# Kernel optimization log

Hardware: AMD Instinct MI355X
Metric: run time of the kernel (lower is better)

Reference implementation:

```python
import jax, jax.numpy as jnp
import numpy as np

N, T, F, H, DEG = 1024, 32, 128, 4, 32
HID, OUT = 512, 64
NNZ = N * DEG
D = F // H


def setup_inputs() -> dict:
    key = jax.random.key(0)
    ks = jax.random.split(key, 40)
    p = lambda i, shape, s=0.05: (jax.random.normal(ks[i], shape, dtype=jnp.float32) * s)
    inp = {
        'A_rows': jnp.repeat(jnp.arange(N, dtype=jnp.int32), DEG),
        'A_cols': jax.random.randint(ks[0], (NNZ,), 0, N, dtype=jnp.int32),
        'A_vals': jax.random.uniform(ks[1], (NNZ,), dtype=jnp.float32) / DEG,
        'X': jax.random.normal(ks[2], (N, T, F), dtype=jnp.float32),
        'W_gcn': p(3, (F, F)),
        'W_ih': p(4, (3 * F, F)), 'W_hh': p(5, (3 * F, F)),
        'b_ih': p(6, (3 * F,)), 'b_hh': p(7, (3 * F,)),
        'in_proj_w': p(8, (3 * F, F)), 'in_proj_b': p(9, (3 * F,)),
        'out_proj_w': p(10, (F, F)), 'out_proj_b': p(11, (F,)),
        'ln1_g': jnp.ones((F,), jnp.float32), 'ln1_b': jnp.zeros((F,), jnp.float32),
        'ln2_g': jnp.ones((F,), jnp.float32), 'ln2_b': jnp.zeros((F,), jnp.float32),
        'lnf_g': jnp.ones((F,), jnp.float32), 'lnf_b': jnp.zeros((F,), jnp.float32),
        'ff1_w': p(12, (HID, F)), 'ff1_b': p(13, (HID,)),
        'ff2_w': p(14, (F, HID)), 'ff2_b': p(15, (F,)),
        'fc1_w': p(16, (HID, T * F)), 'fc1_b': p(17, (HID,)),
        'fc2_w': p(18, (HID, HID)), 'fc2_b': p(19, (HID,)),
        'fc3_w': p(20, (OUT, HID)), 'fc3_b': p(21, (OUT,)),
    }
    return inp


def _pos_encoding():
    # pe[i, t] = sin(t / 10000**(2i/F)) for even t, cos(...) for odd t; constant over feature dim.
    i = jnp.arange(N, dtype=jnp.float32)
    t = jnp.arange(T, dtype=jnp.float32)
    inv = jnp.exp(-(2.0 * i / F) * jnp.log(jnp.float32(10000.0)))  # [N]
    ang = t[None, :] * inv[:, None]                                # [N, T]
    even = (jnp.arange(T) % 2 == 0)[None, :]
    return jnp.where(even, jnp.sin(ang), jnp.cos(ang))             # [N, T]


def _layer_norm(x, g, b, eps=1e-5):
    mu = x.mean(-1, keepdims=True)
    var = ((x - mu) ** 2).mean(-1, keepdims=True)
    return (x - mu) * jax.lax.rsqrt(var + eps) * g + b


def _forward(A_rows, A_cols, A_vals, X, W_gcn, W_ih, W_hh, b_ih, b_hh,
             in_proj_w, in_proj_b, out_proj_w, out_proj_b,
             ln1_g, ln1_b, ln2_g, ln2_b, lnf_g, lnf_b,
             ff1_w, ff1_b, ff2_w, ff2_b,
             fc1_w, fc1_b, fc2_w, fc2_b, fc3_w, fc3_b):
    def spmm(x2d):  # A_hat @ x2d via COO gather + segment-sum
        return jax.ops.segment_sum(A_vals[:, None] * x2d[A_cols], A_rows, num_segments=N)

    def gru_cell(x, h):  # torch GRUCell, gate order [r; z; n]
        gi = x @ W_ih.T + b_ih
        gh = h @ W_hh.T + b_hh
        ir, iz, inn = jnp.split(gi, 3, axis=-1)
        hr, hz, hn = jnp.split(gh, 3, axis=-1)
        r = jax.nn.sigmoid(ir + hr)
        z = jax.nn.sigmoid(iz + hz)
        n = jnp.tanh(inn + r * hn)
        return (1.0 - z) * n + z * h

    # GCN on full [N, T, F] block
    X_tilde = jax.nn.relu(spmm(X.reshape(N, T * F)).reshape(N, T, F) @ W_gcn)

    # sequential GRU + per-step GCN over time
    def step(h, x_t):
        g = gru_cell(x_t, h)                       # [N, F]
        h_new = jax.nn.relu(spmm(g) @ W_gcn)
        return h_new, g

    h0 = jnp.zeros((N, F), X.dtype)
    _, Hs = jax.lax.scan(step, h0, jnp.transpose(X_tilde, (1, 0, 2)))  # [T, N, F]
    Hm = jnp.transpose(Hs, (1, 0, 2)) + _pos_encoding()[:, :, None]    # [N, T, F]

    # TransformerEncoderLayer (post-norm, relu, dropout=0); seq axis = nodes, batch axis = T
    qkv = Hm @ in_proj_w.T + in_proj_b                 # [N, T, 3F]
    q, k, v = jnp.split(qkv, 3, axis=-1)
    q = q.reshape(N, T, H, D) * (1.0 / jnp.sqrt(jnp.float32(D)))
    k = k.reshape(N, T, H, D)
    v = v.reshape(N, T, H, D)
    scores = jnp.einsum('nthd,mthd->thnm', q, k)       # [T, H, N, N]
    attn = jax.nn.softmax(scores, axis=-1)
    ctx = jnp.einsum('thnm,mthd->nthd', attn, v).reshape(N, T, F)
    attn_out = ctx @ out_proj_w.T + out_proj_b
    x1 = _layer_norm(Hm + attn_out, ln1_g, ln1_b)
    ff = jax.nn.relu(x1 @ ff1_w.T + ff1_b) @ ff2_w.T + ff2_b
    x2 = _layer_norm(x1 + ff, ln2_g, ln2_b)
    enc = _layer_norm(x2, lnf_g, lnf_b)                # final encoder norm

    # MLP head
    flat = enc.reshape(N, T * F)
    h1 = jax.nn.relu(flat @ fc1_w.T + fc1_b)
    h2 = jax.nn.relu(h1 @ fc2_w.T + fc2_b)
    return h2 @ fc3_w.T + fc3_b                        # [N, OUT]


def reference(A_rows, A_cols, A_vals, X, W_gcn, W_ih, W_hh, b_ih, b_hh,
              in_proj_w, in_proj_b, out_proj_w, out_proj_b,
              ln1_g, ln1_b, ln2_g, ln2_b, lnf_g, lnf_b,
              ff1_w, ff1_b, ff2_w, ff2_b,
              fc1_w, fc1_b, fc2_w, fc2_b, fc3_w, fc3_b):
    return _forward(A_rows, A_cols, A_vals, X, W_gcn, W_ih, W_hh, b_ih, b_hh,
                    in_proj_w, in_proj_b, out_proj_w, out_proj_b,
                    ln1_g, ln1_b, ln2_g, ln2_b, lnf_g, lnf_b,
                    ff1_w, ff1_b, ff2_w, ff2_b,
                    fc1_w, fc1_b, fc2_w, fc2_b, fc3_w, fc3_b)
```

## Files before the change

### kernel.cpp

```cpp
#include <hip/hip_runtime.h>
#include <hip/hip_bf16.h>
#include <math.h>

#define N_NODES 1024
#define T_STEPS 32
#define F_DIM   128
#define H_HEADS 4
#define D_HEAD  32
#define DEG     32
#define HID     512
#define OUT_DIM 64
#define TF      (T_STEPS * F_DIM)
#define NT      (N_NODES * T_STEPS)
#define F3      (3 * F_DIM)

typedef __attribute__((ext_vector_type(8))) __bf16 bf16x8;
typedef __attribute__((ext_vector_type(4))) float  f32x4;

__device__ __forceinline__ short f2bf(float x) {
    union { float f; unsigned u; } v; v.f = x;
    unsigned r = (v.u + 0x7FFFu + ((v.u >> 16) & 1u)) >> 16;
    return (short)r;
}
__device__ __forceinline__ float bf2f(unsigned short b) {
    union { unsigned u; float f; } v; v.u = ((unsigned)b) << 16; return v.f;
}

__global__ void zero_kernel(float* p, int n) {
    int i = blockIdx.x * 256 + threadIdx.x;
    if (i < n) p[i] = 0.f;
}

template <bool RELU>
__global__ void bias_act(float* __restrict__ C, const float* __restrict__ bias,
                         int P, int total) {
    int i = blockIdx.x * 256 + threadIdx.x;
    if (i < total) {
        float v = C[i] + bias[i & (P - 1)];
        if (RELU) v = fmaxf(v, 0.f);
        C[i] = v;
    }
}

__global__ void prep_weights(const float* __restrict__ W_hh, const float* __restrict__ W_gcn,
                             unsigned short* __restrict__ WhhT_bf,
                             unsigned short* __restrict__ Wg_bf) {
    int idx = blockIdx.x * 256 + threadIdx.x;
    if (idx < F3 * F_DIM) {
        int j = idx / F_DIM;
        int k = idx % F_DIM;
        WhhT_bf[k * F3 + j] = (unsigned short)f2bf(W_hh[idx]);
    }
    if (idx < F_DIM * F_DIM) {
        Wg_bf[idx] = (unsigned short)f2bf(W_gcn[idx]);
    }
}

__global__ void spmm_wide(const int* __restrict__ cols, const float* __restrict__ vals,
                          const float* __restrict__ X, float* __restrict__ Y) {
    int n = blockIdx.y;
    int c = blockIdx.x * 256 + threadIdx.x;
    const int*   ce = cols + n * DEG;
    const float* ve = vals + n * DEG;
    float acc = 0.f;
#pragma unroll
    for (int e = 0; e < DEG; ++e) acc += ve[e] * X[ce[e] * TF + c];
    Y[n * TF + c] = acc;
}

__global__ __launch_bounds__(256) void gates0_kernel(
        const float* __restrict__ GI, const float* __restrict__ b_hh,
        float* __restrict__ g_out, float* __restrict__ Hm) {
    int idx = blockIdx.x * 256 + threadIdx.x;
    int n = idx >> 7, f = idx & 127;
    size_t gib = (size_t)n * T_STEPS * F3;
    float rr = 1.f / (1.f + expf(-(GI[gib + f] + b_hh[f])));
    float zz = 1.f / (1.f + expf(-(GI[gib + 128 + f] + b_hh[128 + f])));
    float nn = tanhf(GI[gib + 256 + f] + rr * b_hh[256 + f]);
    float g  = (1.f - zz) * nn;
    g_out[idx] = g;
    Hm[(size_t)n * T_STEPS * F_DIM + f] = g;
}

__global__ __launch_bounds__(256) void scan_step(
        const int* __restrict__ cols, const float* __restrict__ vals,
        const float* __restrict__ g_in, const unsigned short* __restrict__ Wg_bf,
        const unsigned short* __restrict__ WhhT_bf, const float* __restrict__ b_hh,
        const float* __restrict__ GI, float* __restrict__ g_out,
        float* __restrict__ Hm, int t_next) {
    __shared__ float sp[2][F_DIM];
    __shared__ float hsn[2][F_DIM];
    __shared__ float part[2][F_DIM][8];
    __shared__ float gpart[2][2][F_DIM];
    int tid = threadIdx.x;
    int n0 = blockIdx.x * 2;
    int f = tid & 127, half = tid >> 7;
    float b0 = 0.f, b1 = 0.f;
    int eb = half * 16;
#pragma unroll
    for (int e = 0; e < 16; ++e) {
        int i0 = n0 * DEG + eb + e;
        int i1 = (n0 + 1) * DEG + eb + e;
        b0 += vals[i0] * g_in[cols[i0] * F_DIM + f];
        b1 += vals[i1] * g_in[cols[i1] * F_DIM + f];
    }
    gpart[half][0][f] = b0; gpart[half][1][f] = b1;
    __syncthreads();
    sp[half][f] = gpart[0][half][f] + gpart[1][half][f];
    __syncthreads();
    float c0 = 0.f, c1 = 0.f;
    int kb = half * 64;
#pragma unroll 4
    for (int k = 0; k < 64; ++k) {
        int kk = kb + k;
        float w = bf2f(Wg_bf[kk * F_DIM + f]);
        c0 += sp[0][kk] * w; c1 += sp[1][kk] * w;
    }
    gpart[half][0][f] = c0; gpart[half][1][f] = c1;
    __syncthreads();
    hsn[half][f] = fmaxf(gpart[0][half][f] + gpart[1][half][f], 0.f);
    __syncthreads();
    float a[6] = {0.f, 0.f, 0.f, 0.f, 0.f, 0.f};
#pragma unroll 2
    for (int k = 0; k < 64; ++k) {
        int kk = kb + k;
        const unsigned short* w = WhhT_bf + kk * F3;
        float wr = bf2f(w[f]), wz = bf2f(w[128 + f]), wn = bf2f(w[256 + f]);
        float h0 = hsn[0][kk], h1 = hsn[1][kk];
        a[0] += h0 * wr; a[1] += h0 * wz; a[2] += h0 * wn;
        a[3] += h1 * wr; a[4] += h1 * wz; a[5] += h1 * wn;
    }
#pragma unroll
    for (int i = 0; i < 6; ++i) part[half][f][i] = a[i];
    __syncthreads();
    {
        int node = n0 + half;
        float ghr = part[0][f][half * 3 + 0] + part[1][f][half * 3 + 0] + b_hh[f];
        float ghz = part[0][f][half * 3 + 1] + part[1][f][half * 3 + 1] + b_hh[128 + f];
        float ghn = part[0][f][half * 3 + 2] + part[1][f][half * 3 + 2] + b_hh[256 + f];
        size_t gib = ((size_t)node * T_STEPS + t_next) * F3;
        float hv = hsn[half][f];
        float rr = 1.f / (1.f + expf(-(GI[gib + f] + ghr)));
        float zz = 1.f / (1.f + expf(-(GI[gib + 128 + f] + ghz)));
        float nn = tanhf(GI[gib + 256 + f] + rr * ghn);
        float g  = (1.f - zz) * nn + zz * hv;
        g_out[node * F_DIM + f] = g;
        float inv = __expf(-(float)node * (9.210340371976184f / 64.0f));
        float ang = (float)t_next * inv;
        float pe  = ((t_next & 1) == 0) ? sinf(ang) : cosf(ang);
        Hm[((size_t)node * T_STEPS + t_next) * F_DIM + f] = g + pe;
    }
}

template <bool RELU, bool ABF16, bool BF16OUT>
__global__ __launch_bounds__(256) void mfma_gemm128(const void* __restrict__ Aptr,
                                                    const float* __restrict__ B,
                                                    const float* __restrict__ bias,
                                                    void* __restrict__ Cptr,
                                                    int M, int K, int P) {
    __shared__ short As[128][40];
    __shared__ short Bs[128][40];
    int tid = threadIdx.x;
    int p0 = blockIdx.x * 128, row0 = blockIdx.y * 128;
    int lane = tid & 63, w = tid >> 6, col = lane & 15, quad = lane >> 4;
    int qr = w >> 1, qc = w & 1;
    f32x4 acc[4][4];
#pragma unroll
    for (int j = 0; j < 4; ++j)
#pragma unroll
        for (int jj = 0; jj < 4; ++jj) acc[j][jj] = (f32x4){0.f, 0.f, 0.f, 0.f};

    for (int k0 = 0; k0 < K; k0 += 32) {
        if (ABF16) {
            const short* A = (const short*)Aptr;
#pragma unroll
            for (int i = 0; i < 2; ++i) {
                int idx = tid * 2 + i;
                int r = idx >> 2, c8 = (idx & 3) * 8;
                *(int4*)&As[r][c8] = *(const int4*)(A + (size_t)(row0 + r) * K + k0 + c8);
            }
        } else {
            const float* A = (const float*)Aptr;
#pragma unroll
            for (int i = 0; i < 4; ++i) {
                int idx = tid * 4 + i;
                int r = idx >> 3, c4 = (idx & 7) << 2;
                const float4 f4 = *(const float4*)(A + (size_t)(row0 + r) * K + k0 + c4);
                union { __hip_bfloat162 h2[2]; short4 s4; } u;
                u.h2[0] = __float22bfloat162_rn(make_float2(f4.x, f4.y));
                u.h2[1] = __float22bfloat162_rn(make_float2(f4.z, f4.w));
                *(short4*)&As[r][c4] = u.s4;
            }
        }
#pragma unroll
        for (int i = 0; i < 4; ++i) {
            int idx = tid * 4 + i;
            int r = idx >> 3, c4 = (idx & 7) << 2;
            const float4 f4 = *(const float4*)(B + (size_t)(p0 + r) * K + k0 + c4);
            union { __hip_bfloat162 h2[2]; short4 s4; } u;
            u.h2[0] = __float22bfloat162_rn(make_float2(f4.x, f4.y));
            u.h2[1] = __float22bfloat162_rn(make_float2(f4.z, f4.w));
            *(short4*)&Bs[r][c4] = u.s4;
        }
        __syncthreads();
        bf16x8 af[4], bfr[4];
#pragma unroll
        for (int j = 0; j < 4; ++j) af[j]  = *(const bf16x8*)&As[qr * 64 + j * 16 + col][quad * 8];
#pragma unroll
        for (int j = 0; j < 4; ++j) bfr[j] = *(const bf16x8*)&Bs[qc * 64 + j * 16 + col][quad * 8];
#pragma unroll
        for (int j = 0; j < 4; ++j)
#pragma unroll
            for (int jj = 0; jj < 4; ++jj)
                acc[j][jj] = __builtin_amdgcn_mfma_f32_16x16x32_bf16(af[j], bfr[jj], acc[j][jj], 0, 0, 0);
        __syncthreads();
    }
#pragma unroll
    for (int j = 0; j < 4; ++j) {
#pragma unroll
        for (int jj = 0; jj < 4; ++jj) {
            int cg = p0 + qc * 64 + jj * 16 + col;
            float bvv = bias ? bias[cg] : 0.f;
#pragma unroll
            for (int r = 0; r < 4; ++r) {
                int rg = row0 + qr * 64 + j * 16 + quad * 4 + r;
                float v = acc[j][jj][r] + bvv;
                if (RELU) v = fmaxf(v, 0.f);
                if (BF16OUT) ((short*)Cptr)[(size_t)rg * P + cg] = f2bf(v);
                else         ((float*)Cptr)[(size_t)rg * P + cg] = v;
            }
        }
    }
}

__global__ __launch_bounds__(256) void qkv_gemm128(const float* __restrict__ A,
                                                   const float* __restrict__ B,
                                                   const float* __restrict__ bias,
                                                   short* __restrict__ Qb,
                                                   short* __restrict__ Kb,
                                                   short* __restrict__ Vb) {
    __shared__ short As[128][40];
    __shared__ short Bs[128][40];
    int tid = threadIdx.x;
    int p0 = blockIdx.x * 128, row0 = blockIdx.y * 128;
    int lane = tid & 63, w = tid >> 6, col = lane & 15, quad = lane >> 4;
    int qr = w >> 1, qc = w & 1;
    const int K = F_DIM;
    f32x4 acc[4][4];
#pragma unroll
    for (int j = 0; j < 4; ++j)
#pragma unroll
        for (int jj = 0; jj < 4; ++jj) acc[j][jj] = (f32x4){0.f, 0.f, 0.f, 0.f};

    for (int k0 = 0; k0 < K; k0 += 32) {
#pragma unroll
        for (int i = 0; i < 4; ++i) {
            int idx = tid * 4 + i;
            int r = idx >> 3, c4 = (idx & 7) << 2;
            const float4 f4 = *(const float4*)(A + (size_t)(row0 + r) * K + k0 + c4);
            union { __hip_bfloat162 h2[2]; short4 s4; } u;
            u.h2[0] = __float22bfloat162_rn(make_float2(f4.x, f4.y));
            u.h2[1] = __float22bfloat162_rn(make_float2(f4.z, f4.w));
            *(short4*)&As[r][c4] = u.s4;
        }
#pragma unroll
        for (int i = 0; i < 4; ++i) {
            int idx = tid * 4 + i;
            int r = idx >> 3, c4 = (idx & 7) << 2;
            const float4 f4 = *(const float4*)(B + (size_t)(p0 + r) * K + k0 + c4);
            union { __hip_bfloat162 h2[2]; short4 s4; } u;
            u.h2[0] = __float22bfloat162_rn(make_float2(f4.x, f4.y));
            u.h2[1] = __float22bfloat162_rn(make_float2(f4.z, f4.w));
            *(short4*)&Bs[r][c4] = u.s4;
        }
        __syncthreads();
        bf16x8 af[4], bfr[4];
#pragma unroll
        for (int j = 0; j < 4; ++j) af[j]  = *(const bf16x8*)&As[qr * 64 + j * 16 + col][quad * 8];
#pragma unroll
        for (int j = 0; j < 4; ++j) bfr[j] = *(const bf16x8*)&Bs[qc * 64 + j * 16 + col][quad * 8];
#pragma unroll
        for (int j = 0; j < 4; ++j)
#pragma unroll
            for (int jj = 0; jj < 4; ++jj)
                acc[j][jj] = __builtin_amdgcn_mfma_f32_16x16x32_bf16(af[j], bfr[jj], acc[j][jj], 0, 0, 0);
        __syncthreads();
    }
#pragma unroll
    for (int j = 0; j < 4; ++j) {
#pragma unroll
        for (int jj = 0; jj < 4; ++jj) {
            int cg = p0 + qc * 64 + jj * 16 + col;
            int which = cg >> 7, f = cg & 127;
            int hh = f >> 5, d = f & 31;
            float bv = bias[cg];
#pragma unroll
            for (int r = 0; r < 4; ++r) {
                int rg = row0 + qr * 64 + j * 16 + quad * 4 + r;
                int n = rg >> 5, t = rg & 31;
                int th = t * H_HEADS + hh;
                size_t dst = ((size_t)th * N_NODES + n) * D_HEAD + d;
                float v = acc[j][jj][r] + bv;
                if (which == 0)      Qb[dst] = f2bf(v * 0.17677669529663687f);
                else if (which == 1) Kb[dst] = f2bf(v);
                else                 Vb[dst] = f2bf(v);
            }
        }
    }
}

__global__ __launch_bounds__(256) void vtrans(const short* __restrict__ Vb,
                                              short* __restrict__ VTb) {
    __shared__ short tile[32][36];
    int th = blockIdx.x;
    int n0 = blockIdx.y * 32;
    int tid = threadIdx.x;
    {
        int n_i = tid >> 3, d0 = (tid & 7) * 4;
        *(short4*)&tile[n_i][d0] =
            *(const short4*)(Vb + ((size_t)th * N_NODES + n0 + n_i) * D_HEAD + d0);
    }
    __syncthreads();
    {
        int d = tid >> 3, m0 = (tid & 7) * 4;
        short4 o;
        o.x = tile[m0 + 0][d]; o.y = tile[m0 + 1][d];
        o.z = tile[m0 + 2][d]; o.w = tile[m0 + 3][d];
        *(short4*)(VTb + ((size_t)th * D_HEAD + d) * N_NODES + n0 + m0) = o;
    }
}

__global__ __launch_bounds__(256) void attn_mfma(const short* __restrict__ Qb,
                                                 const short* __restrict__ Kb,
                                                 const short* __restrict__ VTb,
                                                 float* __restrict__ ctx) {
    int th = blockIdx.x;
    int t = th >> 2, hh = th & 3;
    int q0 = blockIdx.y * 64;
    int tid = threadIdx.x;
    int w = tid >> 6, lane = tid & 63;
    int col = lane & 15, quad = lane >> 4;
    __shared__ short    Ks[32][40];
    __shared__ short    Vs[32][40];
    __shared__ unsigned Ps[4][16][20];

    bf16x8 qf = *(const bf16x8*)(Qb + ((size_t)th * N_NODES + q0 + w * 16 + col) * D_HEAD + quad * 8);
    const short* Kbase = Kb  + (size_t)th * (N_NODES * D_HEAD);
    const short* Vbase = VTb + (size_t)th * (D_HEAD * N_NODES);

    int lrw = tid >> 3;
    int lc  = (tid & 7) * 4;
    int kperm = ((lrw & 15) << 1) | (lrw >> 4);

    f32x4 o0 = {0.f, 0.f, 0.f, 0.f}, o1 = {0.f, 0.f, 0.f, 0.f};
    float l0 = 0.f, l1 = 0.f, l2 = 0.f, l3 = 0.f;
    const f32x4 zc = {0.f, 0.f, 0.f, 0.f};

    for (int mt = 0; mt < 32; ++mt) {
        int m0 = mt * 32;
        __syncthreads();
        *(short4*)&Ks[lrw][lc] = *(const short4*)(Kbase + (size_t)(m0 + kperm) * D_HEAD + lc);
        *(short4*)&Vs[lrw][lc] = *(const short4*)(Vbase + (size_t)lrw * N_NODES + m0 + lc);
        __syncthreads();
        bf16x8 k0 = *(const bf16x8*)&Ks[col][quad * 8];
        bf16x8 k1 = *(const bf16x8*)&Ks[col + 16][quad * 8];
        f32x4 s0 = __builtin_amdgcn_mfma_f32_16x16x32_bf16(qf, k0, zc, 0, 0, 0);
        f32x4 s1 = __builtin_amdgcn_mfma_f32_16x16x32_bf16(qf, k1, zc, 0, 0, 0);
        float ps[4][2];
#pragma unroll
        for (int r = 0; r < 4; ++r) {
            ps[r][0] = __expf(fminf(s0[r], 80.f));
            ps[r][1] = __expf(fminf(s1[r], 80.f));
            union { __hip_bfloat162 h; unsigned u; } u;
            u.h = __float22bfloat162_rn(make_float2(ps[r][0], ps[r][1]));
            Ps[w][quad * 4 + r][col] = u.u;
        }
        l0 += ps[0][0] + ps[0][1]; l1 += ps[1][0] + ps[1][1];
        l2 += ps[2][0] + ps[2][1]; l3 += ps[3][0] + ps[3][1];
        __builtin_amdgcn_s_waitcnt(0xC07F);
        bf16x8 pf = *(const bf16x8*)&Ps[w][col][quad * 4];
        bf16x8 v0 = *(const bf16x8*)&Vs[col][quad * 8];
        bf16x8 v1 = *(const bf16x8*)&Vs[col + 16][quad * 8];
        o0 = __builtin_amdgcn_mfma_f32_16x16x32_bf16(pf, v0, o0, 0, 0, 0);
        o1 = __builtin_amdgcn_mfma_f32_16x16x32_bf16(pf, v1, o1, 0, 0, 0);
    }
    float lr[4] = {l0, l1, l2, l3};
#pragma unroll
    for (int r = 0; r < 4; ++r) {
        float s = lr[r];
        s += __shfl_xor(s, 1); s += __shfl_xor(s, 2);
        s += __shfl_xor(s, 4); s += __shfl_xor(s, 8);
        lr[r] = 1.f / s;
    }
#pragma unroll
    for (int r = 0; r < 4; ++r) {
        int n = q0 + w * 16 + quad * 4 + r;
        size_t base = ((size_t)n * T_STEPS + t) * F_DIM + hh * D_HEAD;
        ctx[base + col]      = o0[r] * lr[r];
        ctx[base + 16 + col] = o1[r] * lr[r];
    }
}

__global__ __launch_bounds__(256) void ln_kernel(
        const float* __restrict__ a, const float* __restrict__ resid,
        const float* __restrict__ gamma, const float* __restrict__ beta,
        float* __restrict__ out) {
    int row = blockIdx.x * 4 + (threadIdx.x >> 6);
    int tid = threadIdx.x & 63;
    int base = row * F_DIM;
    float x0 = a[base + tid], x1 = a[base + 64 + tid];
    if (resid) { x0 += resid[base + tid]; x1 += resid[base + 64 + tid]; }
    float s = x0 + x1;
#pragma unroll
    for (int o = 32; o > 0; o >>= 1) s += __shfl_xor(s, o);
    float mu = s * (1.f / 128.f);
    float d0 = x0 - mu, d1 = x1 - mu;
    float v = d0 * d0 + d1 * d1;
#pragma unroll
    for (int o = 32; o > 0; o >>= 1) v += __shfl_xor(v, o);
    float inv = rsqrtf(v * (1.f / 128.f) + 1e-5f);
    out[base + tid]      = d0 * inv * gamma[tid] + beta[tid];
    out[base + 64 + tid] = d1 * inv * gamma[64 + tid] + beta[64 + tid];
}

template <bool TB, bool RELU, bool SPLITK>
__global__ __launch_bounds__(256) void mfma_gemm(const float* __restrict__ A,
                                                 const float* __restrict__ B,
                                                 const float* __restrict__ bias,
                                                 float* __restrict__ C,
                                                 int M, int K, int P, int Kc) {
    __shared__ short As[64][40];
    __shared__ short Bs[64][40];
    int tid = threadIdx.x;
    int p0 = blockIdx.x * 64, row0 = blockIdx.y * 64;
    int k_begin = SPLITK ? blockIdx.z * Kc : 0;
    int k_end   = SPLITK ? k_begin + Kc : K;
    int lane = tid & 63, w = tid >> 6, col = lane & 15, quad = lane >> 4;
    f32x4 acc[4];
#pragma unroll
    for (int j = 0; j < 4; ++j) acc[j] = (f32x4){0.f, 0.f, 0.f, 0.f};

    for (int k0 = k_begin; k0 < k_end; k0 += 32) {
#pragma unroll
        for (int i = 0; i < 2; ++i) {
            int idx = tid * 2 + i;
            int r = idx >> 3, c4 = (idx & 7) << 2;
            const float4 f4 = *(const float4*)(A + (size_t)(row0 + r) * K + k0 + c4);
            union { __hip_bfloat162 h2[2]; short4 s4; } u;
            u.h2[0] = __float22bfloat162_rn(make_float2(f4.x, f4.y));
            u.h2[1] = __float22bfloat162_rn(make_float2(f4.z, f4.w));
            *(short4*)&As[r][c4] = u.s4;
        }
        if (TB) {
#pragma unroll
            for (int i = 0; i < 2; ++i) {
                int idx = tid * 2 + i;
                int r = idx >> 3, c4 = (idx & 7) << 2;
                const float4 f4 = *(const float4*)(B + (size_t)(p0 + r) * K + k0 + c4);
                union { __hip_bfloat162 h2[2]; short4 s4; } u;
                u.h2[0] = __float22bfloat162_rn(make_float2(f4.x, f4.y));
                u.h2[1] = __float22bfloat162_rn(make_float2(f4.z, f4.w));
                *(short4*)&Bs[r][c4] = u.s4;
            }
        } else {
#pragma unroll
            for (int i = 0; i < 2; ++i) {
                int idx = tid * 2 + i;
                int kk = idx >> 4, c4 = (idx & 15) << 2;
                const float4 f4 = *(const float4*)(B + (size_t)(k0 + kk) * P + p0 + c4);
                Bs[c4 + 0][kk] = f2bf(f4.x);
                Bs[c4 + 1][kk] = f2bf(f4.y);
                Bs[c4 + 2][kk] = f2bf(f4.z);
                Bs[c4 + 3][kk] = f2bf(f4.w);
            }
        }
        __syncthreads();
        bf16x8 af = *(const bf16x8*)&As[w * 16 + col][quad * 8];
#pragma unroll
        for (int j = 0; j < 4; ++j) {
            bf16x8 bv = *(const bf16x8*)&Bs[j * 16 + col][quad * 8];
            acc[j] = __builtin_amdgcn_mfma_f32_16x16x32_bf16(af, bv, acc[j], 0, 0, 0);
        }
        __syncthreads();
    }
#pragma unroll
    for (int j = 0; j < 4; ++j) {
        int cg_ = p0 + j * 16 + col;
        float bvv = (!SPLITK && bias) ? bias[cg_] : 0.f;
#pragma unroll
        for (int r = 0; r < 4; ++r) {
            int rg = row0 + w * 16 + quad * 4 + r;
            if (SPLITK) {
                atomicAdd(&C[(size_t)rg * P + cg_], acc[j][r]);
            } else {
                float v = acc[j][r] + bvv;
                if (RELU) v = fmaxf(v, 0.f);
                C[(size_t)rg * P + cg_] = v;
            }
        }
    }
}

extern "C" void kernel_launch(void* const* d_in, const int* in_sizes, int n_in,
                              void* d_out, int out_size, void* d_ws, size_t ws_size,
                              hipStream_t stream) {
    const int*   A_cols     = (const int*)d_in[1];
    const float* A_vals     = (const float*)d_in[2];
    const float* X          = (const float*)d_in[3];
    const float* W_gcn      = (const float*)d_in[4];
    const float* W_ih       = (const float*)d_in[5];
    const float* W_hh       = (const float*)d_in[6];
    const float* b_ih       = (const float*)d_in[7];
    const float* b_hh       = (const float*)d_in[8];
    const float* in_proj_w  = (const float*)d_in[9];
    const float* in_proj_b  = (const float*)d_in[10];
    const float* out_proj_w = (const float*)d_in[11];
    const float* out_proj_b = (const float*)d_in[12];
    const float* ln1_g = (const float*)d_in[13];
    const float* ln1_b = (const float*)d_in[14];
    const float* ln2_g = (const float*)d_in[15];
    const float* ln2_b = (const float*)d_in[16];
    const float* lnf_g = (const float*)d_in[17];
    const float* lnf_b = (const float*)d_in[18];
    const float* ff1_w = (const float*)d_in[19];
    const float* ff1_b = (const float*)d_in[20];
    const float* ff2_w = (const float*)d_in[21];
    const float* ff2_b = (const float*)d_in[22];
    const float* fc1_w = (const float*)d_in[23];
    const float* fc1_b = (const float*)d_in[24];
    const float* fc2_w = (const float*)d_in[25];
    const float* fc2_b = (const float*)d_in[26];
    const float* fc3_w = (const float*)d_in[27];
    const float* fc3_b = (const float*)d_in[28];
    float* out = (float*)d_out;
    float* ws  = (float*)d_ws;

    const size_t o_Hm = 0;
    const size_t o_A  = o_Hm + 4194304;
    const size_t o_B  = o_A + 4194304;
    const size_t o_C  = o_B + 4194304;
    const size_t o_D  = o_C + 12582912;
    const size_t o_WT = o_D + 12582912;
    const size_t o_h  = o_WT + 49152;
    const size_t o_g  = o_h + 131072;
    const size_t o_h1 = o_g + 131072;
    const size_t o_h2 = o_h1 + 524288;

    float* Hm    = ws + o_Hm;
    float* bufA  = ws + o_A;
    float* bufB  = ws + o_B;
    float* bufC  = ws + o_C;
    short* ffh   = (short*)bufC;
    short* Qb    = (short*)(ws + o_D);
    short* Kb    = Qb + 4194304;
    short* VTb   = Kb + 4194304;
    short* Vb    = VTb + 4194304;
    unsigned short* WhhT_bf = (unsigned short*)(ws + o_WT);
    unsigned short* Wg_bf   = WhhT_bf + 49152;
    float* g0    = ws + o_g;
    float* h1    = ws + o_h1;
    float* h2    = ws + o_h2;
    float* g1    = h2;

    spmm_wide<<<dim3(16, 1024), 256, 0, stream>>>(A_cols, A_vals, X, bufA);
    mfma_gemm<false, true, false><<<dim3(2, 512), 256, 0, stream>>>(bufA, W_gcn, nullptr, bufB, NT, F_DIM, F_DIM, 0);
    mfma_gemm128<false, false, false><<<dim3(3, 256), 256, 0, stream>>>(bufB, W_ih, b_ih, bufC, NT, F_DIM, F3);
    prep_weights<<<192, 256, 0, stream>>>(W_hh, W_gcn, WhhT_bf, Wg_bf);
    gates0_kernel<<<512, 256, 0, stream>>>(bufC, b_hh, g0, Hm);
    for (int s = 0; s < T_STEPS - 1; ++s) {
        const float* gi = (s & 1) ? g1 : g0;
        float*       go = (s & 1) ? g0 : g1;
        scan_step<<<512, 256, 0, stream>>>(A_cols, A_vals, gi, Wg_bf, WhhT_bf, b_hh, bufC, go, Hm, s + 1);
    }
    qkv_gemm128<<<dim3(3, 256), 256, 0, stream>>>(Hm, in_proj_w, in_proj_b, Qb, Kb, Vb);
    vtrans<<<dim3(128, 32), 256, 0, stream>>>(Vb, VTb);
    attn_mfma<<<dim3(128, 16), 256, 0, stream>>>(Qb, Kb, VTb, bufA);
    mfma_gemm<true, false, false><<<dim3(2, 512), 256, 0, stream>>>(bufA, out_proj_w, out_proj_b, bufB, NT, F_DIM, F_DIM, 0);
    ln_kernel<<<NT / 4, 256, 0, stream>>>(Hm, bufB, ln1_g, ln1_b, bufA);
    mfma_gemm128<true, false, true><<<dim3(4, 256), 256, 0, stream>>>(bufA, ff1_w, ff1_b, ffh, NT, F_DIM, HID);
    mfma_gemm128<false, true, false><<<dim3(1, 256), 256, 0, stream>>>(ffh, ff2_w, ff2_b, bufB, NT, HID, F_DIM);
    ln_kernel<<<NT / 4, 256, 0, stream>>>(bufA, bufB, ln2_g, ln2_b, Hm);
    ln_kernel<<<NT / 4, 256, 0, stream>>>(Hm, nullptr, lnf_g, lnf_b, bufA);
    zero_kernel<<<2048, 256, 0, stream>>>(h1, 524288);
    mfma_gemm<true, false, true><<<dim3(8, 16, 4), 256, 0, stream>>>(bufA, fc1_w, nullptr, h1, N_NODES, TF, HID, 1024);
    bias_act<true><<<2048, 256, 0, stream>>>(h1, fc1_b, HID, 524288);
    zero_kernel<<<2048, 256, 0, stream>>>(h2, 524288);
    mfma_gemm<true, false, true><<<dim3(8, 16, 4), 256, 0, stream>>>(h1, fc2_w, nullptr, h2, N_NODES, HID, HID, 128);
    bias_act<true><<<2048, 256, 0, stream>>>(h2, fc2_b, HID, 524288);
    zero_kernel<<<256, 256, 0, stream>>>(out, 65536);
    mfma_gemm<true, false, true><<<dim3(1, 16, 8), 256, 0, stream>>>(h2, fc3_w, nullptr, out, N_NODES, HID, OUT_DIM, 64);
    bias_act<false><<<256, 256, 0, stream>>>(out, fc3_b, OUT_DIM, 65536);
}
```

Before: 738.3 us.

## Fuse layernorms, replace split-K atomics with partial buffers, store SpMM output as bf16

The SpMM now writes bf16 output, which the GCN GEMM reads directly through a new bf16 A-path. It also swaps its grid axes. The final two layernorms are fused into one kernel, and the ff2 GEMM moves to the 64-tile GEMM with bf16 input. The split-K head GEMMs now write per-slice partial buffers, and a reduce+bias+relu kernel sums them. This replaces the zero-fill, atomic-add and bias passes. The softmax exp clamp is removed. Together these cut launches, memory traffic and atomics, at some risk of overflow without the clamp.

```diff
diff --git a/kernel.cpp b/kernel.cpp
--- a/kernel.cpp
+++ b/kernel.cpp
@@ -26,22 +26,6 @@
     union { unsigned u; float f; } v; v.u = ((unsigned)b) << 16; return v.f;
 }
 
-__global__ void zero_kernel(float* p, int n) {
-    int i = blockIdx.x * 256 + threadIdx.x;
-    if (i < n) p[i] = 0.f;
-}
-
-template <bool RELU>
-__global__ void bias_act(float* __restrict__ C, const float* __restrict__ bias,
-                         int P, int total) {
-    int i = blockIdx.x * 256 + threadIdx.x;
-    if (i < total) {
-        float v = C[i] + bias[i & (P - 1)];
-        if (RELU) v = fmaxf(v, 0.f);
-        C[i] = v;
-    }
-}
-
 __global__ void prep_weights(const float* __restrict__ W_hh, const float* __restrict__ W_gcn,
                              unsigned short* __restrict__ WhhT_bf,
                              unsigned short* __restrict__ Wg_bf) {
@@ -56,16 +40,29 @@
     }
 }
 
+template <bool RELU>
+__global__ void reduce_bias(const float* __restrict__ part, int nz, int MP,
+                            const float* __restrict__ bias, int P,
+                            float* __restrict__ C) {
+    int i = blockIdx.x * 256 + threadIdx.x;
+    if (i < MP) {
+        float v = bias[i & (P - 1)];
+        for (int z = 0; z < nz; ++z) v += part[(size_t)z * MP + i];
+        if (RELU) v = fmaxf(v, 0.f);
+        C[i] = v;
+    }
+}
+
 __global__ void spmm_wide(const int* __restrict__ cols, const float* __restrict__ vals,
-                          const float* __restrict__ X, float* __restrict__ Y) {
-    int n = blockIdx.y;
-    int c = blockIdx.x * 256 + threadIdx.x;
+                          const float* __restrict__ X, short* __restrict__ Y) {
+    int n = blockIdx.x;
+    int c = blockIdx.y * 256 + threadIdx.x;
     const int*   ce = cols + n * DEG;
     const float* ve = vals + n * DEG;
     float acc = 0.f;
 #pragma unroll
-    for (int e = 0; e < DEG; ++e) acc += ve[e] * X[ce[e] * TF + c];
-    Y[n * TF + c] = acc;
+    for (int e = 0; e < DEG; ++e) acc += ve[e] * X[(size_t)ce[e] * TF + c];
+    Y[(size_t)n * TF + c] = f2bf(acc);
 }
 
 __global__ __launch_bounds__(256) void gates0_kernel(
@@ -369,8 +366,8 @@
         float ps[4][2];
 #pragma unroll
         for (int r = 0; r < 4; ++r) {
-            ps[r][0] = __expf(fminf(s0[r], 80.f));
-            ps[r][1] = __expf(fminf(s1[r], 80.f));
+            ps[r][0] = __expf(s0[r]);
+            ps[r][1] = __expf(s1[r]);
             union { __hip_bfloat162 h; unsigned u; } u;
             u.h = __float22bfloat162_rn(make_float2(ps[r][0], ps[r][1]));
             Ps[w][quad * 4 + r][col] = u.u;
@@ -423,8 +420,42 @@
     out[base + 64 + tid] = d1 * inv * gamma[64 + tid] + beta[64 + tid];
 }
 
-template <bool TB, bool RELU, bool SPLITK>
-__global__ __launch_bounds__(256) void mfma_gemm(const float* __restrict__ A,
+__global__ __launch_bounds__(256) void ln2_lnf_kernel(
+        const float* __restrict__ a, const float* __restrict__ resid,
+        const float* __restrict__ g2, const float* __restrict__ b2,
+        const float* __restrict__ gf, const float* __restrict__ bfp,
+        float* __restrict__ out) {
+    int row = blockIdx.x * 4 + (threadIdx.x >> 6);
+    int tid = threadIdx.x & 63;
+    int base = row * F_DIM;
+    float x0 = a[base + tid] + resid[base + tid];
+    float x1 = a[base + 64 + tid] + resid[base + 64 + tid];
+    float s = x0 + x1;
+#pragma unroll
+    for (int o = 32; o > 0; o >>= 1) s += __shfl_xor(s, o);
+    float mu = s * (1.f / 128.f);
+    float d0 = x0 - mu, d1 = x1 - mu;
+    float v = d0 * d0 + d1 * d1;
+#pragma unroll
+    for (int o = 32; o > 0; o >>= 1) v += __shfl_xor(v, o);
+    float inv = rsqrtf(v * (1.f / 128.f) + 1e-5f);
+    float y0 = d0 * inv * g2[tid] + b2[tid];
+    float y1 = d1 * inv * g2[64 + tid] + b2[64 + tid];
+    s = y0 + y1;
+#pragma unroll
+    for (int o = 32; o > 0; o >>= 1) s += __shfl_xor(s, o);
+    mu = s * (1.f / 128.f);
+    d0 = y0 - mu; d1 = y1 - mu;
+    v = d0 * d0 + d1 * d1;
+#pragma unroll
+    for (int o = 32; o > 0; o >>= 1) v += __shfl_xor(v, o);
+    inv = rsqrtf(v * (1.f / 128.f) + 1e-5f);
+    out[base + tid]      = d0 * inv * gf[tid] + bfp[tid];
+    out[base + 64 + tid] = d1 * inv * gf[64 + tid] + bfp[64 + tid];
+}
+
+template <bool TB, bool RELU, bool SPLITK, bool ABF16>
+__global__ __launch_bounds__(256) void mfma_gemm(const void* __restrict__ Aptr,
                                                  const float* __restrict__ B,
                                                  const float* __restrict__ bias,
                                                  float* __restrict__ C,
@@ -441,15 +472,22 @@
     for (int j = 0; j < 4; ++j) acc[j] = (f32x4){0.f, 0.f, 0.f, 0.f};
 
     for (int k0 = k_begin; k0 < k_end; k0 += 32) {
-#pragma unroll
-        for (int i = 0; i < 2; ++i) {
-            int idx = tid * 2 + i;
-            int r = idx >> 3, c4 = (idx & 7) << 2;
-            const float4 f4 = *(const float4*)(A + (size_t)(row0 + r) * K + k0 + c4);
-            union { __hip_bfloat162 h2[2]; short4 s4; } u;
-            u.h2[0] = __float22bfloat162_rn(make_float2(f4.x, f4.y));
-            u.h2[1] = __float22bfloat162_rn(make_float2(f4.z, f4.w));
-            *(short4*)&As[r][c4] = u.s4;
+        if (ABF16) {
+            const short* A = (const short*)Aptr;
+            int r = tid >> 2, c8 = (tid & 3) * 8;
+            *(int4*)&As[r][c8] = *(const int4*)(A + (size_t)(row0 + r) * K + k0 + c8);
+        } else {
+            const float* A = (const float*)Aptr;
+#pragma unroll
+            for (int i = 0; i < 2; ++i) {
+                int idx = tid * 2 + i;
+                int r = idx >> 3, c4 = (idx & 7) << 2;
+                const float4 f4 = *(const float4*)(A + (size_t)(row0 + r) * K + k0 + c4);
+                union { __hip_bfloat162 h2[2]; short4 s4; } u;
+                u.h2[0] = __float22bfloat162_rn(make_float2(f4.x, f4.y));
+                u.h2[1] = __float22bfloat162_rn(make_float2(f4.z, f4.w));
+                *(short4*)&As[r][c4] = u.s4;
+            }
         }
         if (TB) {
 #pragma unroll
@@ -483,6 +521,7 @@
         }
         __syncthreads();
     }
+    size_t zoff = SPLITK ? (size_t)blockIdx.z * M * P : 0;
 #pragma unroll
     for (int j = 0; j < 4; ++j) {
         int cg_ = p0 + j * 16 + col;
@@ -490,13 +529,9 @@
 #pragma unroll
         for (int r = 0; r < 4; ++r) {
             int rg = row0 + w * 16 + quad * 4 + r;
-            if (SPLITK) {
-                atomicAdd(&C[(size_t)rg * P + cg_], acc[j][r]);
-            } else {
-                float v = acc[j][r] + bvv;
-                if (RELU) v = fmaxf(v, 0.f);
-                C[(size_t)rg * P + cg_] = v;
-            }
+            float v = acc[j][r] + bvv;
+            if (!SPLITK && RELU) v = fmaxf(v, 0.f);
+            C[zoff + (size_t)rg * P + cg_] = v;
         }
     }
 }
@@ -548,6 +583,7 @@
 
     float* Hm    = ws + o_Hm;
     float* bufA  = ws + o_A;
+    short* Xs    = (short*)bufA;
     float* bufB  = ws + o_B;
     float* bufC  = ws + o_C;
     short* ffh   = (short*)bufC;
@@ -555,6 +591,7 @@
     short* Kb    = Qb + 4194304;
     short* VTb   = Kb + 4194304;
     short* Vb    = VTb + 4194304;
+    float* partbuf = ws + o_D;
     unsigned short* WhhT_bf = (unsigned short*)(ws + o_WT);
     unsigned short* Wg_bf   = WhhT_bf + 49152;
     float* g0    = ws + o_g;
@@ -562,8 +599,8 @@
     float* h2    = ws + o_h2;
     float* g1    = h2;
 
-    spmm_wide<<<dim3(16, 1024), 256, 0, stream>>>(A_cols, A_vals, X, bufA);
-    mfma_gemm<false, true, false><<<dim3(2, 512), 256, 0, stream>>>(bufA, W_gcn, nullptr, bufB, NT, F_DIM, F_DIM, 0);
+    spmm_wide<<<dim3(1024, 16), 256, 0, stream>>>(A_cols, A_vals, X, Xs);
+    mfma_gemm<false, true, false, true><<<dim3(2, 512), 256, 0, stream>>>(Xs, W_gcn, nullptr, bufB, NT, F_DIM, F_DIM, 0);
     mfma_gemm128<false, false, false><<<dim3(3, 256), 256, 0, stream>>>(bufB, W_ih, b_ih, bufC, NT, F_DIM, F3);
     prep_weights<<<192, 256, 0, stream>>>(W_hh, W_gcn, WhhT_bf, Wg_bf);
     gates0_kernel<<<512, 256, 0, stream>>>(bufC, b_hh, g0, Hm);
@@ -575,19 +612,15 @@
     qkv_gemm128<<<dim3(3, 256), 256, 0, stream>>>(Hm, in_proj_w, in_proj_b, Qb, Kb, Vb);
     vtrans<<<dim3(128, 32), 256, 0, stream>>>(Vb, VTb);
     attn_mfma<<<dim3(128, 16), 256, 0, stream>>>(Qb, Kb, VTb, bufA);
-    mfma_gemm<true, false, false><<<dim3(2, 512), 256, 0, stream>>>(bufA, out_proj_w, out_proj_b, bufB, NT, F_DIM, F_DIM, 0);
+    mfma_gemm<true, false, false, false><<<dim3(2, 512), 256, 0, stream>>>(bufA, out_proj_w, out_proj_b, bufB, NT, F_DIM, F_DIM, 0);
     ln_kernel<<<NT / 4, 256, 0, stream>>>(Hm, bufB, ln1_g, ln1_b, bufA);
     mfma_gemm128<true, false, true><<<dim3(4, 256), 256, 0, stream>>>(bufA, ff1_w, ff1_b, ffh, NT, F_DIM, HID);
-    mfma_gemm128<false, true, false><<<dim3(1, 256), 256, 0, stream>>>(ffh, ff2_w, ff2_b, bufB, NT, HID, F_DIM);
-    ln_kernel<<<NT / 4, 256, 0, stream>>>(bufA, bufB, ln2_g, ln2_b, Hm);
-    ln_kernel<<<NT / 4, 256, 0, stream>>>(Hm, nullptr, lnf_g, lnf_b, bufA);
-    zero_kernel<<<2048, 256, 0, stream>>>(h1, 524288);
-    mfma_gemm<true, false, true><<<dim3(8, 16, 4), 256, 0, stream>>>(bufA, fc1_w, nullptr, h1, N_NODES, TF, HID, 1024);
-    bias_act<true><<<2048, 256, 0, stream>>>(h1, fc1_b, HID, 524288);
-    zero_kernel<<<2048, 256, 0, stream>>>(h2, 524288);
-    mfma_gemm<true, false, true><<<dim3(8, 16, 4), 256, 0, stream>>>(h1, fc2_w, nullptr, h2, N_NODES, HID, HID, 128);
-    bias_act<true><<<2048, 256, 0, stream>>>(h2, fc2_b, HID, 524288);
-    zero_kernel<<<256, 256, 0, stream>>>(out, 65536);
-    mfma_gemm<true, false, true><<<dim3(1, 16, 8), 256, 0, stream>>>(h2, fc3_w, nullptr, out, N_NODES, HID, OUT_DIM, 64);
-    bias_act<false><<<256, 256, 0, stream>>>(out, fc3_b, OUT_DIM, 65536);
-}
+    mfma_gemm<true, false, false, true><<<dim3(2, 512), 256, 0, stream>>>(ffh, ff2_w, ff2_b, bufB, NT, HID, F_DIM, 0);
+    ln2_lnf_kernel<<<NT / 4, 256, 0, stream>>>(bufA, bufB, ln2_g, ln2_b, lnf_g, lnf_b, bufA);
+    mfma_gemm<true, false, true, false><<<dim3(8, 16, 4), 256, 0, stream>>>(bufA, fc1_w, nullptr, partbuf, N_NODES, TF, HID, 1024);
+    reduce_bias<true><<<2048, 256, 0, stream>>>(partbuf, 4, 524288, fc1_b, HID, h1);
+    mfma_gemm<true, false, true, false><<<dim3(8, 16, 4), 256, 0, stream>>>(h1, fc2_w, nullptr, partbuf, N_NODES, HID, HID, 128);
+    reduce_bias<true><<<2048, 256, 0, stream>>>(partbuf, 4, 524288, fc2_b, HID, h2);
+    mfma_gemm<true, false, true, false><<<dim3(1, 16, 8), 256, 0, stream>>>(h2, fc3_w, nullptr, partbuf, N_NODES, HID, OUT_DIM, 64);
+    reduce_bias<false><<<256, 256, 0, stream>>>(partbuf, 8, 65536, fc3_b, OUT_DIM, out);
+}
```

Result: no change. 739.9 us (+0.2%).
